# Kernel tuning notes

Measured on AMD Instinct MI355X. Metric: run time of the kernel, lower is better.

The kernel has to match this reference:

```python
import jax, jax.numpy as jnp
import numpy as np

G = 8      # deform_groups
KK = 9     # 3x3 kernel positions


def conv2d(x, w, b, pad):
    out = jax.lax.conv_general_dilated(
        x, w, window_strides=(1, 1), padding=[(pad, pad), (pad, pad)],
        dimension_numbers=('NCHW', 'OIHW', 'NCHW'))
    return out + b[None, :, None, None]


def deform_conv(x, offset, w):
    # x: [B,C,H,W], offset: [B, G*2*KK, H, W] (mmcv layout: per group, per kernel pos k: (dy, dx)),
    # w: [Cout, C, 3, 3]. Zero padding outside image (mmcv DeformConv2d semantics), pad=1, stride=1.
    B, C, H, W = x.shape
    Cg = C // G
    off = offset.reshape(B, G, KK, 2, H, W)
    dy, dx = off[:, :, :, 0], off[:, :, :, 1]            # [B,G,KK,H,W]
    ky = jnp.repeat(jnp.arange(3) - 1, 3)                # kernel row offsets, (kh,kw) order
    kx = jnp.tile(jnp.arange(3) - 1, 3)
    sy = dy + jnp.arange(H)[None, :, None] + ky[:, None, None]   # [B,G,KK,H,W]
    sx = dx + jnp.arange(W)[None, None, :] + kx[:, None, None]
    y0 = jnp.floor(sy); x0 = jnp.floor(sx)
    wy = sy - y0; wx = sx - x0
    y0i = y0.astype(jnp.int32); x0i = x0.astype(jnp.int32)
    xg = x.reshape(B, G, Cg, H * W)

    def gather(yi, xi):
        valid = ((yi >= 0) & (yi < H) & (xi >= 0) & (xi < W)).astype(x.dtype)
        idx = jnp.clip(yi, 0, H - 1) * W + jnp.clip(xi, 0, W - 1)
        vals = jnp.take_along_axis(xg, idx.reshape(B, G, 1, KK * H * W), axis=3)
        return vals.reshape(B, G, Cg, KK, H, W) * valid[:, :, None]

    v00 = gather(y0i, x0i)
    v01 = gather(y0i, x0i + 1)
    v10 = gather(y0i + 1, x0i)
    v11 = gather(y0i + 1, x0i + 1)
    wy_ = wy[:, :, None]; wx_ = wx[:, :, None]           # [B,G,1,KK,H,W]
    samp = (v00 * (1 - wy_) * (1 - wx_) + v01 * (1 - wy_) * wx_
            + v10 * wy_ * (1 - wx_) + v11 * wy_ * wx_)   # [B,G,Cg,KK,H,W]
    wr = w.reshape(w.shape[0], G, Cg, KK)
    return jnp.einsum('ogck,bgckhw->bohw', wr, samp)


def reference(x, w_off1, b_off1, w_off2, b_off2, w_align1, w_alignf):
    B, T, C, H, W = x.shape
    # AvgPool3d kernel/stride [1,2,2]: spatial 2x2 mean per frame
    x2 = x.reshape(B, T, C, H // 2, 2, W // 2, 2).mean(axis=(4, 6))
    tc = T // 2
    fc1 = x[:, tc]
    fc2 = x2[:, tc]
    outs = []
    for i in range(T):
        if i == tc:
            outs.append(fc1)
            continue
        fn2 = x2[:, i]
        off2 = conv2d(jnp.concatenate([fn2, fc2], axis=1), w_off2, b_off2, pad=1)
        # bilinear upsample x2, align_corners=False (half-pixel, matches jax.image.resize)
        off2_us = jax.image.resize(off2, (B, off2.shape[1], H, W), method='bilinear') * 2.0
        fn1 = x[:, i]
        z1 = deform_conv(fn1, off2_us, w_align1)
        off1 = conv2d(jnp.concatenate([z1, fc1], axis=1), w_off1, b_off1, pad=2) + off2_us
        outs.append(deform_conv(fn1, off1, w_alignf))
    return jnp.stack(outs, axis=1)


def setup_inputs() -> dict:
    key = jax.random.key(0)
    ks = jax.random.split(key, 8)
    B, T, C, H, W = 2, 5, 64, 128, 128
    offC = G * 2 * KK  # 144
    return {
        'x': jax.random.normal(ks[0], (B, T, C, H, W), dtype=jnp.float32),
        # offset predictor weights kept small so sampled offsets are modest/realistic
        'w_off1': jax.random.normal(ks[1], (offC, 2 * C, 5, 5), dtype=jnp.float32) * 0.005,
        'b_off1': jnp.zeros((offC,), dtype=jnp.float32),
        'w_off2': jax.random.normal(ks[2], (offC, 2 * C, 3, 3), dtype=jnp.float32) * 0.005,
        'b_off2': jnp.zeros((offC,), dtype=jnp.float32),
        'w_align1': jax.random.normal(ks[3], (C, C, 3, 3), dtype=jnp.float32) * 0.05,
        'w_alignf': jax.random.normal(ks[4], (C, C, 3, 3), dtype=jnp.float32) * 0.05,
    }
```

## Files before the change

kernel.cpp:

```cpp
#include <hip/hip_runtime.h>
#include <cstdint>

#define BB 2
#define TT 5
#define CC 64
#define HH 128
#define WW 128
#define GG 8
#define KKD 9
#define OFFC 144
#define H2 64
#define W2 64
#define TCF 2
#define HW (HH*WW)
#define HW2 (H2*W2)
#define PLANE1 278784
#define PLANE0 69696

typedef __attribute__((ext_vector_type(4))) short short4v;
typedef __attribute__((ext_vector_type(8))) short short8;
typedef __attribute__((ext_vector_type(4))) float floatx4;
typedef __attribute__((ext_vector_type(16))) float floatx16;

static __device__ __forceinline__ unsigned short f2bf(float f) {
    unsigned int u = __float_as_uint(f);
    unsigned int r = (u + 0x7fffu + ((u >> 16) & 1u)) >> 16;
    return (unsigned short)r;
}

typedef __attribute__((address_space(1))) const unsigned int g_u32;
typedef __attribute__((address_space(3))) unsigned int l_u32;
static __device__ __forceinline__ void async16(const short* g, short* l) {
    __builtin_amdgcn_global_load_lds((g_u32*)g, (l_u32*)l, 16, 0, 0);
}

__global__ void wswzD_k(const float* __restrict__ w, short* __restrict__ ws) {
    int idx = blockIdx.x * 256 + threadIdx.x;
    if (idx >= 36864) return;
    int j = idx & 7;
    int lane = (idx >> 3) & 63;
    int tile = (idx >> 9) & 1;
    int chunk = idx >> 10;
    int ck = chunk * 16 + (lane >> 5) * 8 + j;
    int oc = tile * 32 + (lane & 31);
    int cin = ck / 9;
    int kt = ck - cin * 9;
    ws[idx] = (short)f2bf(w[((size_t)oc * 64 + cin) * 9 + kt]);
}

template <int TAPS>
__global__ void wswz_k(const float* __restrict__ w, short* __restrict__ ws) {
    int idx = blockIdx.x * 256 + threadIdx.x;
    if (idx >= 8 * TAPS * 5 * 512) return;
    int jj = idx & 7;
    int lane = (idx >> 3) & 63;
    int rest = idx >> 9;
    int ocF = rest % 5;
    int ct = rest / 5;
    int tap = ct % TAPS;
    int chunk = ct / TAPS;
    int oc = ocF * 32 + (lane & 31);
    int cin = chunk * 16 + (lane >> 5) * 8 + jj;
    float v = 0.f;
    if (oc < OFFC) v = w[((size_t)oc * 128 + cin) * TAPS + tap];
    ws[idx] = (short)f2bf(v);
}

__global__ void avgpool_k(const float* __restrict__ x, short* __restrict__ x2T) {
    __shared__ float sL[64 * 17];
    const int h2 = blockIdx.x;
    const int chunk = blockIdx.y;
    const int img = blockIdx.z;
    const int tid = threadIdx.x;
    const float* base = x + ((size_t)img * 64 + chunk * 16) * HW + (size_t)(2 * h2) * WW;
#pragma unroll
    for (int it = 0; it < 4; ++it) {
        int e = it * 256 + tid;
        int cin = e >> 6, w2 = e & 63;
        const float* sp = base + (size_t)cin * HW + 2 * w2;
        sL[w2 * 17 + cin] = 0.25f * (sp[0] + sp[1] + sp[WW] + sp[WW + 1]);
    }
    __syncthreads();
    int w2 = tid >> 2, cg = tid & 3;
    short4v sv;
#pragma unroll
    for (int q = 0; q < 4; ++q) sv[q] = (short)f2bf(sL[w2 * 17 + cg * 4 + q]);
    *(short4v*)&x2T[((size_t)img * 4 + chunk) * PLANE0 +
                    ((size_t)(h2 + 1) * 66 + (w2 + 1)) * 16 + cg * 4] = sv;
}

__global__ void xtrans_k(const float* __restrict__ x, short* __restrict__ xT) {
    __shared__ float sL[128 * 17];
    const int row = blockIdx.x;
    const int chunk = blockIdx.y;
    const int b = blockIdx.z;
    const int tid = threadIdx.x;
    const float* base = x + ((size_t)(b * 5 + TCF) * 64 + chunk * 16) * HW + (size_t)row * WW;
#pragma unroll
    for (int it = 0; it < 8; ++it) {
        int e = it * 256 + tid;
        int cin = e >> 7, col = e & 127;
        sL[col * 17 + cin] = base[(size_t)cin * HW + col];
    }
    __syncthreads();
    int col = tid >> 1, half = tid & 1;
    short8 sv;
#pragma unroll
    for (int q = 0; q < 8; ++q) sv[q] = (short)f2bf(sL[col * 17 + half * 8 + q]);
    *(short8*)&xT[((size_t)b * 4 + chunk) * PLANE1 +
                  ((size_t)(row + 2) * 132 + (col + 2)) * 16 + half * 8] = sv;
}

__global__ void xgt_k(const float* __restrict__ x, float* __restrict__ xg) {
    __shared__ float sL[128 * 9];
    const int row = blockIdx.x;
    const int g = blockIdx.y;
    const int bj = blockIdx.z;
    const int b = bj >> 2;
    const int j = bj & 3;
    const int i = j + (j >= 2 ? 1 : 0);
    const int tid = threadIdx.x;
    const float* base = x + ((size_t)(b * TT + i) * CC + g * 8) * HW + (size_t)row * WW;
#pragma unroll
    for (int it = 0; it < 4; ++it) {
        int e = it * 256 + tid;
        int cin = e >> 7, col = e & 127;
        sL[col * 9 + cin] = base[(size_t)cin * HW + col];
    }
    __syncthreads();
    int col = tid >> 1, half = tid & 1;
    floatx4 v;
#pragma unroll
    for (int q = 0; q < 4; ++q) v[q] = sL[col * 9 + half * 4 + q];
    *(floatx4*)&xg[(((size_t)(bj * 8 + g) * HW + row * WW + col) << 3) + half * 4] = v;
}

static __device__ __forceinline__ void conv0_body(
    const short* __restrict__ srcAT,
    const short* __restrict__ wswz, const float* __restrict__ bias,
    float* __restrict__ out) {
    constexpr int KS = 3;
    constexpr int IM = 64;
    constexpr int PD = IM + KS - 1;
    constexpr int TAPS = KS * KS;
    constexpr int OROWS = 4;
    constexpr int SROWS = OROWS + KS - 1;
    constexpr int PLANE = PD * PD * 16;
    constexpr int SLAB16 = SROWS * PD * 2;
    constexpr int BUFSH = SROWS * PD * 16;

    extern __shared__ __align__(16) short stg[];

    const int bj = blockIdx.z;
    const int b = bj >> 2;
    const int j = bj & 3;
    const int i = j + (j >= 2 ? 1 : 0);
    const int y0 = blockIdx.x * OROWS;
    const int tid = threadIdx.x;
    const int wave = tid >> 6;
    const int lane = tid & 63;
    const int l31 = lane & 31;
    const int quad = lane >> 5;
    const int wrb = wave >> 1;
    const int wc0 = (wave & 1) * 32;

    const short* srcA = srcAT + (size_t)((b * 5 + i) * 4) * PLANE;
    const short* srcB = srcAT + (size_t)((b * 5 + TCF) * 4) * PLANE;

    floatx16 acc[5];
#pragma unroll
    for (int o = 0; o < 5; ++o)
#pragma unroll
        for (int g = 0; g < 16; ++g) acc[o][g] = 0.f;

    auto stage = [&](int c, int sIdx) {
        const short* plane = (c < 4) ? (srcA + (size_t)c * PLANE)
                                     : (srcB + (size_t)(c - 4) * PLANE);
        const short* srcRow = plane + (size_t)y0 * (PD * 16);
        short* dst = stg + (size_t)sIdx * BUFSH;
        for (int base = wave * 64; base < SLAB16; base += 512) {
            int b2 = min(base, SLAB16 - 64);
            async16(srcRow + (size_t)(b2 + lane) * 8, dst + (size_t)b2 * 8);
        }
    };

    stage(0, 0);
    for (int c = 0; c < 8; ++c) {
        __syncthreads();
        if (c < 7) stage(c + 1, (c + 1) & 1);
        const short* sbuf = stg + (size_t)(c & 1) * BUFSH;
        const short* wpc = wswz + (size_t)c * TAPS * 2560 + lane * 8;
#pragma unroll 5
        for (int tap = 0; tap < TAPS; ++tap) {
            const int ky = tap / KS, kx = tap - ky * KS;
            short8 wf[5];
            const short* wp = wpc + (size_t)tap * 2560;
#pragma unroll
            for (int o = 0; o < 5; ++o) wf[o] = *(const short8*)(wp + o * 512);
            short8 pf = *(const short8*)(sbuf +
                ((size_t)(wrb + ky) * PD + (wc0 + kx + l31)) * 16 + quad * 8);
#pragma unroll
            for (int o = 0; o < 5; ++o)
                acc[o] = __builtin_amdgcn_mfma_f32_32x32x16_bf16(wf[o], pf, acc[o], 0, 0, 0);
        }
    }

    const size_t imgBase = (size_t)bj * OFFC * (IM * IM);
    const size_t rowAddr = imgBase + (size_t)(y0 + wrb) * IM + wc0 + l31;
#pragma unroll
    for (int o = 0; o < 5; ++o) {
        const int rmax = (o == 4) ? 8 : 16;
#pragma unroll
        for (int r = 0; r < 16; ++r) {
            if (r >= rmax) break;
            int oc = o * 32 + (r & 3) + 8 * (r >> 2) + 4 * quad;
            float v = acc[o][r] + bias[oc];
            out[rowAddr + (size_t)oc * (IM * IM)] = v;
        }
    }
}

__global__ __launch_bounds__(512) void convmf0_k(
    const short* __restrict__ srcAT,
    const short* __restrict__ wswz, const float* __restrict__ bias,
    float* __restrict__ out) {
    conv0_body(srcAT, wswz, bias, out);
}

template <int OCNT, int OBASE>
static __device__ __forceinline__ void conv1_body(
    const short* __restrict__ srcAT, const short* __restrict__ srcBT,
    const short* __restrict__ wswz, const float* __restrict__ bias,
    const float* __restrict__ addend, float* __restrict__ out) {
    constexpr int KS = 5;
    constexpr int IM = 128;
    constexpr int PD = IM + KS - 1;
    constexpr int TAPS = KS * KS;
    constexpr int FR = 2;
    constexpr int OROWS = 2;
    constexpr int NT = 256;
    constexpr int SROWS = OROWS + KS - 1;
    constexpr int PLANE = PD * PD * 16;
    constexpr int SLAB16 = SROWS * PD * 2;
    constexpr int BUFSH = SROWS * PD * 16;

    extern __shared__ __align__(16) short stg[];

    const int bj = blockIdx.z;
    const int b = bj >> 2;
    const int y0 = blockIdx.x * OROWS;
    const int tid = threadIdx.x;
    const int wave = tid >> 6;
    const int lane = tid & 63;
    const int l31 = lane & 31;
    const int quad = lane >> 5;
    const int wrb = wave >> 1;
    const int wc0 = (wave & 1) * 64;

    const short* srcA = srcAT + (size_t)(bj * 4) * PLANE;
    const short* srcB = srcBT + (size_t)(b * 4) * PLANE;

    floatx16 acc[FR][OCNT];
#pragma unroll
    for (int f = 0; f < FR; ++f)
#pragma unroll
        for (int o = 0; o < OCNT; ++o)
#pragma unroll
            for (int g = 0; g < 16; ++g) acc[f][o][g] = 0.f;

    auto stage = [&](int c, int sIdx) {
        const short* plane = (c < 4) ? (srcA + (size_t)c * PLANE)
                                     : (srcB + (size_t)(c - 4) * PLANE);
        const short* srcRow = plane + (size_t)y0 * (PD * 16);
        short* dst = stg + (size_t)sIdx * BUFSH;
        for (int base = wave * 64; base < SLAB16; base += NT) {
            int b2 = min(base, SLAB16 - 64);
            async16(srcRow + (size_t)(b2 + lane) * 8, dst + (size_t)b2 * 8);
        }
    };

    stage(0, 0);
    for (int c = 0; c < 8; ++c) {
        __syncthreads();
        if (c < 7) stage(c + 1, (c + 1) & 1);
        const short* sbuf = stg + (size_t)(c & 1) * BUFSH;
        const short* wpc = wswz + (size_t)c * TAPS * 2560 + lane * 8 + OBASE * 512;
#pragma unroll 5
        for (int tap = 0; tap < TAPS; ++tap) {
            const int ky = tap / KS, kx = tap - ky * KS;
            short8 wf[OCNT];
            const short* wp = wpc + (size_t)tap * 2560;
#pragma unroll
            for (int o = 0; o < OCNT; ++o) wf[o] = *(const short8*)(wp + o * 512);
            short8 pf[FR];
#pragma unroll
            for (int f = 0; f < FR; ++f)
                pf[f] = *(const short8*)(sbuf +
                    ((size_t)(wrb + ky) * PD + (wc0 + f * 32 + kx + l31)) * 16 + quad * 8);
#pragma unroll
            for (int o = 0; o < OCNT; ++o)
#pragma unroll
                for (int f = 0; f < FR; ++f)
                    acc[f][o] = __builtin_amdgcn_mfma_f32_32x32x16_bf16(wf[o], pf[f],
                                                                        acc[f][o], 0, 0, 0);
        }
    }

    const size_t imgBase = (size_t)bj * OFFC * (IM * IM);
#pragma unroll
    for (int f = 0; f < FR; ++f) {
        const size_t rowAddr = imgBase + (size_t)(y0 + wrb) * IM + wc0 + f * 32 + l31;
#pragma unroll
        for (int o = 0; o < OCNT; ++o) {
            const int rmax = ((OBASE + o) == 4) ? 8 : 16;
#pragma unroll
            for (int r = 0; r < 16; ++r) {
                if (r >= rmax) break;
                int oc = (OBASE + o) * 32 + (r & 3) + 8 * (r >> 2) + 4 * quad;
                float v = acc[f][o][r] + bias[oc];
                size_t a = rowAddr + (size_t)oc * (IM * IM);
                out[a] = v + addend[a];
            }
        }
    }
}

__global__ __launch_bounds__(256)
__attribute__((amdgpu_waves_per_eu(3, 3))) void convmf1_k(
    const short* __restrict__ srcAT, const short* __restrict__ srcBT,
    const short* __restrict__ wswz, const float* __restrict__ bias,
    const float* __restrict__ addend, float* __restrict__ out) {
    if (blockIdx.y == 0)
        conv1_body<3, 0>(srcAT, srcBT, wswz, bias, addend, out);
    else
        conv1_body<2, 3>(srcAT, srcBT, wswz, bias, addend, out);
}

__global__ void upsample_k(const float* __restrict__ off2, float* __restrict__ off2u) {
    int idx = blockIdx.x * 256 + threadIdx.x;
    int ox = idx & 127;
    int oy = (idx >> 7) & 127;
    int p = idx >> 14;
    const float* sp = off2 + (size_t)p * HW2;
    float sy = 0.5f * oy - 0.25f;
    float sx = 0.5f * ox - 0.25f;
    float y0f = floorf(sy), x0f = floorf(sx);
    int y0 = (int)y0f, x0 = (int)x0f;
    float fy = sy - y0f, fx = sx - x0f;
    int y0c = max(y0, 0), y1c = min(y0 + 1, 63);
    int x0c = max(x0, 0), x1c = min(x0 + 1, 63);
    float v00 = sp[y0c * 64 + x0c], v01 = sp[y0c * 64 + x1c];
    float v10 = sp[y1c * 64 + x0c], v11 = sp[y1c * 64 + x1c];
    float v = v00 * (1.f - fy) * (1.f - fx) + v01 * (1.f - fy) * fx +
              v10 * fy * (1.f - fx) + v11 * fy * fx;
    off2u[idx] = 2.0f * v;
}

#define SROW 584
__global__ __launch_bounds__(256)
__attribute__((amdgpu_waves_per_eu(4, 4))) void dconv_k(
    const float* __restrict__ xg,
    const float* __restrict__ off,
    const short* __restrict__ wsw,
    float* __restrict__ out, short* __restrict__ z1T, int outMode) {
    const int bj = blockIdx.x;
    const int b = bj >> 2;
    const int j = bj & 3;
    const int i = j + (j >= 2 ? 1 : 0);
    const int seg = blockIdx.y;
    const int y = seg >> 2;
    const int x0 = (seg & 3) << 5;
    const int tid = threadIdx.x;

    __shared__ short sS[32 * SROW];
    float* Pbuf = (float*)sS;

    const float* offp = off + (size_t)bj * OFFC * HW + y * WW + x0;

    {
        const int g = tid >> 5;
        const int px = tid & 31;
        short* srow = sS + px * SROW + g * 72;
        const float* xgp = xg + ((size_t)(bj * 8 + g)) * ((size_t)HW * 8);
        const float* offg = offp + (size_t)(g * 18) * HW + px;
#pragma unroll 1
        for (int kg = 0; kg < 3; ++kg) {
            const int kyy = kg - 1;
            const float fyrow = (float)(y + kyy);
#pragma unroll
            for (int kk = 0; kk < 3; ++kk) {
                const int k = kg * 3 + kk;
                float dy = offg[(size_t)(k * 2) * HW];
                float dx = offg[(size_t)(k * 2 + 1) * HW];
                const int kxx = kk - 1;
                float sy = fyrow + dy;
                float sx = (float)(x0 + px + kxx) + dx;
                float y0f = floorf(sy), x0f = floorf(sx);
                int iy = (int)y0f, ix = (int)x0f;
                float wy = sy - y0f, wx = sx - x0f;
                bool yv0 = (iy >= 0) & (iy < HH);
                bool yv1 = (iy + 1 >= 0) & (iy + 1 < HH);
                bool xv0 = (ix >= 0) & (ix < WW);
                bool xv1 = (ix + 1 >= 0) & (ix + 1 < WW);
                float w00 = (yv0 && xv0) ? (1.f - wy) * (1.f - wx) : 0.f;
                float w01 = (yv0 && xv1) ? (1.f - wy) * wx : 0.f;
                float w10 = (yv1 && xv0) ? wy * (1.f - wx) : 0.f;
                float w11 = (yv1 && xv1) ? wy * wx : 0.f;
                int iy0 = min(max(iy, 0), HH - 1);
                int iy1 = min(max(iy + 1, 0), HH - 1);
                int ix0 = min(max(ix, 0), WW - 1);
                int ix1 = min(max(ix + 1, 0), WW - 1);
                const float* p00 = xgp + ((size_t)(iy0 * WW + ix0) << 3);
                const float* p01 = xgp + ((size_t)(iy0 * WW + ix1) << 3);
                const float* p10 = xgp + ((size_t)(iy1 * WW + ix0) << 3);
                const float* p11 = xgp + ((size_t)(iy1 * WW + ix1) << 3);
                floatx4 a00 = *(const floatx4*)p00, b00 = *(const floatx4*)(p00 + 4);
                floatx4 a01 = *(const floatx4*)p01, b01 = *(const floatx4*)(p01 + 4);
                floatx4 a10 = *(const floatx4*)p10, b10 = *(const floatx4*)(p10 + 4);
                floatx4 a11 = *(const floatx4*)p11, b11 = *(const floatx4*)(p11 + 4);
#pragma unroll
                for (int c = 0; c < 4; ++c) {
                    float v = a00[c] * w00 + a01[c] * w01 + a10[c] * w10 + a11[c] * w11;
                    srow[c * 9 + k] = (short)f2bf(v);
                    float v2 = b00[c] * w00 + b01[c] * w01 + b10[c] * w10 + b11[c] * w11;
                    srow[(c + 4) * 9 + k] = (short)f2bf(v2);
                }
            }
        }
    }
    __syncthreads();

    const int wv = tid >> 6;
    const int lane = tid & 63;
    const int tile = wv >> 1;
    const int kw = wv & 1;
    floatx16 acc;
#pragma unroll
    for (int g = 0; g < 16; ++g) acc[g] = 0.f;

    const short* aBase = sS + (lane & 31) * SROW + (lane >> 5) * 8;
    const short* bBase = wsw + ((size_t)tile * 64 + lane) * 8;
    for (int chunk = kw * 18; chunk < kw * 18 + 18; ++chunk) {
        short8 af = *(const short8*)(aBase + chunk * 16);
        short8 bf = *(const short8*)(bBase + (size_t)chunk * 1024);
        acc = __builtin_amdgcn_mfma_f32_32x32x16_bf16(af, bf, acc, 0, 0, 0);
    }

    __syncthreads();
    {
        const int n = lane & 31;
#pragma unroll
        for (int g = 0; g < 16; ++g) {
            int m = (g & 3) + 8 * (g >> 2) + 4 * (lane >> 5);
            Pbuf[wv * 1056 + m * 33 + n] = acc[g];
        }
    }
    __syncthreads();

    if (outMode == 0) {
        const int chunk = tid >> 6;
        const int px = (tid >> 1) & 31;
        const int half = tid & 1;
        const int t2 = chunk >> 1;
        const int n0 = (chunk & 1) * 16 + half * 8;
        short8 sv;
#pragma unroll
        for (int q = 0; q < 8; ++q) {
            float v = Pbuf[(t2 * 2) * 1056 + px * 33 + n0 + q] +
                      Pbuf[(t2 * 2 + 1) * 1056 + px * 33 + n0 + q];
            sv[q] = (short)f2bf(v);
        }
        *(short8*)&z1T[((size_t)bj * 4 + chunk) * PLANE1 +
                       ((size_t)(y + 2) * 132 + (x0 + 2 + px)) * 16 + half * 8] = sv;
    } else {
        const size_t planeBase = (size_t)(b * TT + i) * CC * HW;
        const size_t rowBase = planeBase + (size_t)y * WW + x0;
#pragma unroll
        for (int rep = 0; rep < 8; ++rep) {
            int elem = rep * 256 + tid;
            int oc = elem >> 5;
            int px = elem & 31;
            int t = oc >> 5;
            int n = oc & 31;
            float v = Pbuf[(t * 2) * 1056 + px * 33 + n] +
                      Pbuf[(t * 2 + 1) * 1056 + px * 33 + n];
            out[rowBase + (size_t)oc * HW + px] = v;
        }
    }
}

__global__ void copy_center_k(const float* __restrict__ x, float* __restrict__ out) {
    int idx = blockIdx.x * 256 + threadIdx.x;
    int b = idx >> 18;
    int rem = idx & 262143;
    size_t o = (((size_t)(b * TT + TCF) * CC * HW) >> 2) + rem;
    ((float4*)out)[o] = ((const float4*)x)[o];
}

extern "C" void kernel_launch(void* const* d_in, const int* in_sizes, int n_in,
                              void* d_out, int out_size, void* d_ws, size_t ws_size,
                              hipStream_t stream) {
    const float* x = (const float*)d_in[0];
    const float* w_off1 = (const float*)d_in[1];
    const float* b_off1 = (const float*)d_in[2];
    const float* w_off2 = (const float*)d_in[3];
    const float* b_off2 = (const float*)d_in[4];
    const float* w_align1 = (const float*)d_in[5];
    const float* w_alignf = (const float*)d_in[6];
    float* out = (float*)d_out;
    float* ws = (float*)d_ws;

    float* off2 = ws;
    float* off2u = ws + 4718592;
    float* off1 = ws + 23592960;
    short* z1T = (short*)(ws + 42467328);
    short* xT = (short*)(ws + 46927872);
    short* x2T = (short*)(ws + 48043008);
    short* wsD1 = (short*)(ws + 49436928);
    short* wsDf = (short*)(ws + 49455360);
    short* w2s = (short*)(ws + 49473792);
    short* w1s = (short*)(ws + 49565952);
    float* xg = ws + 49821952;

    hipMemsetAsync((void*)z1T, 0, 27878400, stream);

    wswzD_k<<<144, 256, 0, stream>>>(w_align1, wsD1);
    wswzD_k<<<144, 256, 0, stream>>>(w_alignf, wsDf);
    wswz_k<9><<<720, 256, 0, stream>>>(w_off2, w2s);
    wswz_k<25><<<2000, 256, 0, stream>>>(w_off1, w1s);

    avgpool_k<<<dim3(64, 4, 10), 256, 0, stream>>>(x, x2T);
    xtrans_k<<<dim3(128, 4, 2), 256, 0, stream>>>(x, xT);
    xgt_k<<<dim3(128, 8, 8), 256, 0, stream>>>(x, xg);

    convmf0_k<<<dim3(16, 1, 8), 512, 25344, stream>>>(x2T, w2s, b_off2, off2);
    upsample_k<<<73728, 256, 0, stream>>>(off2, off2u);
    dconv_k<<<dim3(8, 512), 256, 0, stream>>>(xg, off2u, wsD1, nullptr, z1T, 0);
    convmf1_k<<<dim3(64, 2, 8), 256, 50688, stream>>>(z1T, xT, w1s, b_off1,
                                                      off2u, off1);
    dconv_k<<<dim3(8, 512), 256, 0, stream>>>(xg, off1, wsDf, out, nullptr, 1);
    copy_center_k<<<2048, 256, 0, stream>>>(x, out);
}
```

Measured before the change: 582.4 us.

## Restructure 5x5 offset conv to stage weights in LDS and cover all outputs per block

The 5x5 offset-predictor MFMA conv no longer splits output channels across two blocks. Each 512-thread block now computes all 5 output-channel fragments, with one 32-column fragment per wave. Weights are double-buffered into LDS in tap quarters alongside the input slab, replacing per-lane global weight loads, so the input slab is staged once instead of twice. The cost is a much larger LDS footprint (about 120 KB), which limits occupancy, plus more barriers per channel chunk.

```diff
diff --git a/kernel.cpp b/kernel.cpp
--- a/kernel.cpp
+++ b/kernel.cpp
@@ -227,24 +227,23 @@
     conv0_body(srcAT, wswz, bias, out);
 }
 
-template <int OCNT, int OBASE>
-static __device__ __forceinline__ void conv1_body(
+__global__ __launch_bounds__(512) void convmf1_k(
     const short* __restrict__ srcAT, const short* __restrict__ srcBT,
     const short* __restrict__ wswz, const float* __restrict__ bias,
     const float* __restrict__ addend, float* __restrict__ out) {
     constexpr int KS = 5;
     constexpr int IM = 128;
     constexpr int PD = IM + KS - 1;
-    constexpr int TAPS = KS * KS;
-    constexpr int FR = 2;
     constexpr int OROWS = 2;
-    constexpr int NT = 256;
     constexpr int SROWS = OROWS + KS - 1;
     constexpr int PLANE = PD * PD * 16;
     constexpr int SLAB16 = SROWS * PD * 2;
     constexpr int BUFSH = SROWS * PD * 16;
-
-    extern __shared__ __align__(16) short stg[];
+    constexpr int WQ = 7 * 2560;
+
+    extern __shared__ __align__(16) short lds[];
+    short* pbuf = lds;
+    short* wbuf = lds + 2 * BUFSH;
 
     const int bj = blockIdx.z;
     const int b = bj >> 2;
@@ -254,86 +253,87 @@
     const int lane = tid & 63;
     const int l31 = lane & 31;
     const int quad = lane >> 5;
-    const int wrb = wave >> 1;
-    const int wc0 = (wave & 1) * 64;
+    const int wrb = wave >> 2;
+    const int wc0 = (wave & 3) * 32;
 
     const short* srcA = srcAT + (size_t)(bj * 4) * PLANE;
     const short* srcB = srcBT + (size_t)(b * 4) * PLANE;
 
-    floatx16 acc[FR][OCNT];
-#pragma unroll
-    for (int f = 0; f < FR; ++f)
-#pragma unroll
-        for (int o = 0; o < OCNT; ++o)
-#pragma unroll
-            for (int g = 0; g < 16; ++g) acc[f][o][g] = 0.f;
-
-    auto stage = [&](int c, int sIdx) {
+    floatx16 acc[5];
+#pragma unroll
+    for (int o = 0; o < 5; ++o)
+#pragma unroll
+        for (int g = 0; g < 16; ++g) acc[o][g] = 0.f;
+
+    auto stageP = [&](int c, int sIdx) {
         const short* plane = (c < 4) ? (srcA + (size_t)c * PLANE)
                                      : (srcB + (size_t)(c - 4) * PLANE);
         const short* srcRow = plane + (size_t)y0 * (PD * 16);
-        short* dst = stg + (size_t)sIdx * BUFSH;
-        for (int base = wave * 64; base < SLAB16; base += NT) {
+        short* dst = pbuf + (size_t)sIdx * BUFSH;
+        for (int base = wave * 64; base < SLAB16; base += 512) {
             int b2 = min(base, SLAB16 - 64);
             async16(srcRow + (size_t)(b2 + lane) * 8, dst + (size_t)b2 * 8);
         }
     };
-
-    stage(0, 0);
+    auto stageW = [&](int c, int qoff, int qn, int sIdx) {
+        const short* src = wswz + (size_t)c * 64000 + (size_t)qoff * 2560;
+        short* dst = wbuf + (size_t)sIdx * WQ;
+        const int n16 = qn * 320;
+        for (int base = wave * 64; base < n16; base += 512) {
+            int b2 = min(base, n16 - 64);
+            async16(src + (size_t)(b2 + lane) * 8, dst + (size_t)b2 * 8);
+        }
+    };
+
+    constexpr int QOFF[4] = {0, 7, 13, 19};
+    constexpr int QN[4] = {7, 6, 6, 6};
+
+    stageP(0, 0);
+    stageW(0, 0, 7, 0);
     for (int c = 0; c < 8; ++c) {
-        __syncthreads();
-        if (c < 7) stage(c + 1, (c + 1) & 1);
-        const short* sbuf = stg + (size_t)(c & 1) * BUFSH;
-        const short* wpc = wswz + (size_t)c * TAPS * 2560 + lane * 8 + OBASE * 512;
-#pragma unroll 5
-        for (int tap = 0; tap < TAPS; ++tap) {
-            const int ky = tap / KS, kx = tap - ky * KS;
-            short8 wf[OCNT];
-            const short* wp = wpc + (size_t)tap * 2560;
-#pragma unroll
-            for (int o = 0; o < OCNT; ++o) wf[o] = *(const short8*)(wp + o * 512);
-            short8 pf[FR];
-#pragma unroll
-            for (int f = 0; f < FR; ++f)
-                pf[f] = *(const short8*)(sbuf +
-                    ((size_t)(wrb + ky) * PD + (wc0 + f * 32 + kx + l31)) * 16 + quad * 8);
-#pragma unroll
-            for (int o = 0; o < OCNT; ++o)
-#pragma unroll
-                for (int f = 0; f < FR; ++f)
-                    acc[f][o] = __builtin_amdgcn_mfma_f32_32x32x16_bf16(wf[o], pf[f],
-                                                                        acc[f][o], 0, 0, 0);
+#pragma unroll
+        for (int q = 0; q < 4; ++q) {
+            __syncthreads();
+            if (!(c == 7 && q == 3)) {
+                const int nc = (q == 3) ? c + 1 : c;
+                const int nq = (q == 3) ? 0 : q + 1;
+                stageW(nc, QOFF[nq], QN[nq], (q + 1) & 1);
+            }
+            if (q == 0 && c < 7) stageP(c + 1, (c + 1) & 1);
+            const short* sbuf = pbuf + (size_t)(c & 1) * BUFSH;
+            const short* wb = wbuf + (size_t)(q & 1) * WQ + lane * 8;
+#pragma unroll
+            for (int t = 0; t < QN[q]; ++t) {
+                const int tap = QOFF[q] + t;
+                const int ky = tap / KS, kx = tap - ky * KS;
+                short8 wf[5];
+#pragma unroll
+                for (int o = 0; o < 5; ++o)
+                    wf[o] = *(const short8*)(wb + (t * 5 + o) * 512);
+                short8 pf = *(const short8*)(sbuf +
+                    ((size_t)(wrb + ky) * PD + (wc0 + kx + l31)) * 16 + quad * 8);
+#pragma unroll
+                for (int o = 0; o < 5; ++o)
+                    acc[o] = __builtin_amdgcn_mfma_f32_32x32x16_bf16(wf[o], pf,
+                                                                     acc[o], 0, 0, 0);
+            }
         }
     }
 
     const size_t imgBase = (size_t)bj * OFFC * (IM * IM);
-#pragma unroll
-    for (int f = 0; f < FR; ++f) {
-        const size_t rowAddr = imgBase + (size_t)(y0 + wrb) * IM + wc0 + f * 32 + l31;
-#pragma unroll
-        for (int o = 0; o < OCNT; ++o) {
-            const int rmax = ((OBASE + o) == 4) ? 8 : 16;
-#pragma unroll
-            for (int r = 0; r < 16; ++r) {
-                if (r >= rmax) break;
-                int oc = (OBASE + o) * 32 + (r & 3) + 8 * (r >> 2) + 4 * quad;
-                float v = acc[f][o][r] + bias[oc];
-                size_t a = rowAddr + (size_t)oc * (IM * IM);
-                out[a] = v + addend[a];
-            }
-        }
-    }
-}
-
-__global__ __launch_bounds__(256)
-__attribute__((amdgpu_waves_per_eu(3, 3))) void convmf1_k(
-    const short* __restrict__ srcAT, const short* __restrict__ srcBT,
-    const short* __restrict__ wswz, const float* __restrict__ bias,
-    const float* __restrict__ addend, float* __restrict__ out) {
-    if (blockIdx.y == 0)
-        conv1_body<3, 0>(srcAT, srcBT, wswz, bias, addend, out);
-    else
-        conv1_body<2, 3>(srcAT, srcBT, wswz, bias, addend, out);
+    const size_t rowAddr = imgBase + (size_t)(y0 + wrb) * IM + wc0 + l31;
+#pragma unroll
+    for (int o = 0; o < 5; ++o) {
+        const int rmax = (o == 4) ? 8 : 16;
+#pragma unroll
+        for (int r = 0; r < 16; ++r) {
+            if (r >= rmax) break;
+            int oc = o * 32 + (r & 3) + 8 * (r >> 2) + 4 * quad;
+            float v = acc[o][r] + bias[oc];
+            size_t a = rowAddr + (size_t)oc * (IM * IM);
+            out[a] = v + addend[a];
+        }
+    }
 }
 
 __global__ void upsample_k(const float* __restrict__ off2, float* __restrict__ off2u) {
@@ -536,8 +536,8 @@
     convmf0_k<<<dim3(16, 1, 8), 512, 25344, stream>>>(x2T, w2s, b_off2, off2);
     upsample_k<<<73728, 256, 0, stream>>>(off2, off2u);
     dconv_k<<<dim3(8, 512), 256, 0, stream>>>(xg, off2u, wsD1, nullptr, z1T, 0);
-    convmf1_k<<<dim3(64, 2, 8), 256, 50688, stream>>>(z1T, xT, w1s, b_off1,
-                                                      off2u, off1);
+    convmf1_k<<<dim3(64, 1, 8), 512, 122368, stream>>>(z1T, xT, w1s, b_off1,
+                                                       off2u, off1);
     dconv_k<<<dim3(8, 512), 256, 0, stream>>>(xg, off1, wsDf, out, nullptr, 1);
     copy_center_k<<<2048, 256, 0, stream>>>(x, out);
 }
```

New measurement: 473.2 us. 1.23x faster.
